# Kernel optimization log

Measured on AMD Instinct MI355X. Metric: run time of the kernel, lower is better.

## Reference

```python
import jax, jax.numpy as jnp
import numpy as np


def _apply_rope(x, rope):
    # x: (B, T, D); rope: (T, D//2, 2) broadcast over batch
    B, T, D = x.shape
    x_ = x.reshape(B, T, D // 2, 2)
    cos, sin = rope[..., 0], rope[..., 1]
    xr, xi = x_[..., 0], x_[..., 1]
    rotr = xr * cos - xi * sin
    roti = xr * sin + xi * cos
    return jnp.stack([rotr, roti], axis=-1).reshape(B, T, D)


def setup_inputs() -> dict:
    key = jax.random.key(0)
    k1, k2, k3, k4 = jax.random.split(key, 4)
    B, T, D, H = 2, 2048, 1024, 16
    x = jax.random.normal(k1, (B, T, D), dtype=jnp.float32)
    rope = jax.random.normal(k2, (T, D // 2, 2), dtype=jnp.float32)
    w_qkv = jax.random.normal(k3, (3 * D, D), dtype=jnp.float32) * (1.0 / np.sqrt(D))
    w_proj = jax.random.normal(k4, (D, D), dtype=jnp.float32) * (1.0 / np.sqrt(D))
    return {"x": x, "rope": rope, "w_qkv": w_qkv, "w_proj": w_proj}


def reference(x, rope, w_qkv, w_proj):
    B, T, D = x.shape
    H = 16
    dk = D // H
    qkv = jnp.einsum("btd,ed->bte", x, w_qkv)  # (B, T, 3D)
    q, k, v = jnp.split(qkv, 3, axis=-1)
    q = _apply_rope(q, rope)
    k = _apply_rope(k, rope)
    # split heads: (B, H, T, dk)
    q = q.reshape(B, T, H, dk).transpose(0, 2, 1, 3)
    k = k.reshape(B, T, H, dk).transpose(0, 2, 1, 3)
    v = v.reshape(B, T, H, dk).transpose(0, 2, 1, 3)
    att = jnp.einsum("bhqd,bhkd->bhqk", q, k) / jnp.sqrt(jnp.float32(dk)).astype(x.dtype)
    att = jax.nn.softmax(att, axis=-1)
    out = jnp.einsum("bhqk,bhkd->bhqd", att, v)
    out = out.transpose(0, 2, 1, 3).reshape(B, T, D)
    return jnp.einsum("btd,ed->bte", out, w_proj)
```

## Files before the change

kernel.cpp:

```cpp
#include <hip/hip_runtime.h>

typedef _Float16 f16;
typedef _Float16 f16x2 __attribute__((ext_vector_type(2)));
typedef _Float16 f16x4 __attribute__((ext_vector_type(4)));
typedef _Float16 f16x8 __attribute__((ext_vector_type(8)));
typedef float    f32x2 __attribute__((ext_vector_type(2)));
typedef float    f32x4 __attribute__((ext_vector_type(4)));
typedef short    s16x4 __attribute__((ext_vector_type(4)));

#define GLDS16(gptr, lptr)                                                     \
  __builtin_amdgcn_global_load_lds(                                            \
      (const __attribute__((address_space(1))) void*)(gptr),                   \
      (__attribute__((address_space(3))) void*)(lptr), 16, 0, 0)

#define S_BARRIER() __builtin_amdgcn_s_barrier()
#define FENCE() asm volatile("" ::: "memory")
#define WAIT_VM8() asm volatile("s_waitcnt vmcnt(8)" ::: "memory")
#define WAIT_VM0() asm volatile("s_waitcnt vmcnt(0)" ::: "memory")
#define WAIT_LGKM0() asm volatile("s_waitcnt lgkmcnt(0)" ::: "memory")

__device__ inline short f32_to_bf16_rne(float f) {
  unsigned u = __builtin_bit_cast(unsigned, f);
  return (short)((u + 0x7FFFu + ((u >> 16) & 1u)) >> 16);
}

__global__ __launch_bounds__(256) void k_cast3(const float* __restrict__ a,
                                               const float* __restrict__ b,
                                               const float* __restrict__ c,
                                               f16* __restrict__ oa,
                                               f16* __restrict__ ob,
                                               f16* __restrict__ oc) {
  int i = blockIdx.x * 256 + threadIdx.x;
  const float* src;
  f16* dst;
  int off;
  if (i < 1048576) { src = a; dst = oa; off = i; }
  else if (i < 1835008) { src = b; dst = ob; off = i - 1048576; }
  else { src = c; dst = oc; off = i - 1835008; }
  f32x4 v = ((const f32x4*)src)[off];
  f16x4 h;
  h[0] = (f16)v[0]; h[1] = (f16)v[1]; h[2] = (f16)v[2]; h[3] = (f16)v[3];
  ((f16x4*)dst)[off] = h;
}

__global__ __launch_bounds__(256, 4) void k_gemm_qkv(
    const f16* __restrict__ A, const f16* __restrict__ B,
    const float* __restrict__ rope, f16* __restrict__ qh,
    f16* __restrict__ kh, short* __restrict__ vt) {
  const int K = 1024;
  __shared__ f16 sA[128 * 64];
  __shared__ f16 sB[128 * 64];
  const int tid = threadIdx.x;
  const int wave = tid >> 6, lane = tid & 63;
  const int lr = lane & 15, lq = lane >> 4;
  const int lr7 = lr & 7;
  const int wm = (wave >> 1) * 64, wn = (wave & 1) * 64;
  const size_t m0 = (size_t)blockIdx.x * 128, n0 = (size_t)blockIdx.y * 128;

  f32x4 acc[4][4] = {};

  const int sw8 = ((tid & 7) ^ ((tid >> 3) & 7)) * 8;
  const f16* ga = A + (m0 + (tid >> 3)) * (size_t)K + sw8;
  const f16* gb = B + (n0 + (tid >> 3)) * (size_t)K + sw8;

  for (int k0 = 0; k0 < K; k0 += 64) {
    __syncthreads();
#pragma unroll
    for (int r = 0; r < 4; ++r) {
      GLDS16(ga + (size_t)(r * 32) * K + k0, (char*)sA + r * 4096 + wave * 1024);
      GLDS16(gb + (size_t)(r * 32) * K + k0, (char*)sB + r * 4096 + wave * 1024);
    }
    __syncthreads();

#pragma unroll
    for (int kk = 0; kk < 2; ++kk) {
      f16x8 af[4], bf[4];
#pragma unroll
      for (int i = 0; i < 4; ++i)
        af[i] = *(const f16x8*)&sA[(wm + i * 16 + lr) * 64 +
                                   (((kk * 4 + lq) ^ lr7) * 8)];
#pragma unroll
      for (int j = 0; j < 4; ++j)
        bf[j] = *(const f16x8*)&sB[(wn + j * 16 + lr) * 64 +
                                   (((kk * 4 + lq) ^ lr7) * 8)];
#pragma unroll
      for (int i = 0; i < 4; ++i)
#pragma unroll
        for (int j = 0; j < 4; ++j)
          acc[i][j] = __builtin_amdgcn_mfma_f32_16x16x32_f16(af[i], bf[j],
                                                             acc[i][j], 0, 0, 0);
    }
  }

  const int region = (int)(n0 >> 10);
  if (region == 2) {
#pragma unroll
    for (int i = 0; i < 4; ++i)
#pragma unroll
      for (int j = 0; j < 4; ++j) {
        int e = (int)(n0 + wn + j * 16 + lr) - 2048;
        int h = e >> 6, c = e & 63;
        int m = (int)(m0 + wm + i * 16 + lq * 4);
        int b = m >> 11, t0 = m & 2047;
        s16x4 o;
#pragma unroll
        for (int r = 0; r < 4; ++r) o[r] = f32_to_bf16_rne(acc[i][j][r]);
        *(s16x4*)&vt[(((size_t)(b * 16 + h)) * 64 + c) * 2048 + t0] = o;
      }
  } else {
    const float scl = region == 0 ? 0.1803368801111204f : 1.0f;
    f16* dst = region == 0 ? qh : kh;
    const int odd = lr & 1;
#pragma unroll
    for (int i = 0; i < 4; ++i)
#pragma unroll
      for (int j = 0; j < 4; ++j) {
        int e = ((int)(n0 + wn + j * 16 + lr)) & 1023;
        int h = e >> 6, c = e & 63, p = e >> 1;
        int mb = (int)(m0 + wm + i * 16 + lq * 4);
        int b = mb >> 11;
#pragma unroll
        for (int r = 0; r < 4; ++r) {
          int t = (mb + r) & 2047;
          float v = acc[i][j][r];
          float partner = __shfl_xor(v, 1);
          f32x2 cs = *(const f32x2*)&rope[((size_t)t * 512 + p) * 2];
          float out = odd ? (partner * cs[1] + v * cs[0])
                          : (v * cs[0] - partner * cs[1]);
          dst[(((size_t)(b * 16 + h)) * 2048 + t) * 64 + c] = (f16)(out * scl);
        }
      }
  }
}

__global__ __launch_bounds__(256, 4) void k_gemm_bt(const f16* __restrict__ A,
                                                    const f16* __restrict__ B,
                                                    float* __restrict__ C,
                                                    int M, int N, int K) {
  __shared__ f16 sA[128 * 64];
  __shared__ f16 sB[128 * 64];
  const int tid = threadIdx.x;
  const int wave = tid >> 6, lane = tid & 63;
  const int lr = lane & 15, lq = lane >> 4;
  const int lr7 = lr & 7;
  const int wm = (wave >> 1) * 64, wn = (wave & 1) * 64;
  const size_t m0 = (size_t)blockIdx.x * 128, n0 = (size_t)blockIdx.y * 128;

  f32x4 acc[4][4] = {};

  const int sw8 = ((tid & 7) ^ ((tid >> 3) & 7)) * 8;
  const f16* ga = A + (m0 + (tid >> 3)) * (size_t)K + sw8;
  const f16* gb = B + (n0 + (tid >> 3)) * (size_t)K + sw8;

  for (int k0 = 0; k0 < K; k0 += 64) {
    __syncthreads();
#pragma unroll
    for (int r = 0; r < 4; ++r) {
      GLDS16(ga + (size_t)(r * 32) * K + k0, (char*)sA + r * 4096 + wave * 1024);
      GLDS16(gb + (size_t)(r * 32) * K + k0, (char*)sB + r * 4096 + wave * 1024);
    }
    __syncthreads();

#pragma unroll
    for (int kk = 0; kk < 2; ++kk) {
      f16x8 af[4], bf[4];
#pragma unroll
      for (int i = 0; i < 4; ++i)
        af[i] = *(const f16x8*)&sA[(wm + i * 16 + lr) * 64 +
                                   (((kk * 4 + lq) ^ lr7) * 8)];
#pragma unroll
      for (int j = 0; j < 4; ++j)
        bf[j] = *(const f16x8*)&sB[(wn + j * 16 + lr) * 64 +
                                   (((kk * 4 + lq) ^ lr7) * 8)];
#pragma unroll
      for (int i = 0; i < 4; ++i)
#pragma unroll
        for (int j = 0; j < 4; ++j)
          acc[i][j] = __builtin_amdgcn_mfma_f32_16x16x32_f16(af[i], bf[j],
                                                             acc[i][j], 0, 0, 0);
    }
  }

#pragma unroll
  for (int i = 0; i < 4; ++i)
#pragma unroll
    for (int j = 0; j < 4; ++j)
#pragma unroll
      for (int r = 0; r < 4; ++r)
        C[(m0 + wm + i * 16 + lq * 4 + r) * (size_t)N + n0 + wn + j * 16 + lr] =
            acc[i][j][r];
}

__global__ __launch_bounds__(256, 2) void k_attn(const f16* __restrict__ Qp,
                                                 const f16* __restrict__ Kp,
                                                 const short* __restrict__ Vt,
                                                 f16* __restrict__ Op) {
  __shared__ f16 sQ[128 * 64];
  __shared__ f16 sKV[2 * 16384];
  const int tid = threadIdx.x, wave = tid >> 6, lane = tid & 63;
  const int lr = lane & 15, lq = lane >> 4;
  const int lr7 = lr & 7;
  const int bh = blockIdx.x, qt = blockIdx.y;
  const size_t base = (size_t)bh * 2048 * 64;

  const int sw8 = ((tid & 7) ^ ((tid >> 3) & 7)) * 8;
  const int sw16 = ((tid & 15) ^ ((tid >> 4) & 15)) * 8;

  auto stage_kv = [&](int jcc, int d) {
    const f16* gk = Kp + base + (size_t)jcc * 128 * 64;
    const short* gv = Vt + base + (size_t)jcc * 128;
    char* bK = (char*)sKV + d * 32768;
    char* bV = bK + 16384;
#pragma unroll
    for (int r = 0; r < 4; ++r) {
      GLDS16(gk + (size_t)(r * 32 + (tid >> 3)) * 64 + sw8,
             bK + r * 4096 + wave * 1024);
      GLDS16(gv + (size_t)(r * 16 + (tid >> 4)) * 2048 + sw16,
             bV + r * 4096 + wave * 1024);
    }
  };

  const f16* gq = Qp + base + (size_t)qt * 128 * 64;
#pragma unroll
  for (int r = 0; r < 4; ++r)
    GLDS16(gq + (size_t)(r * 32 + (tid >> 3)) * 64 + sw8,
           (char*)sQ + r * 4096 + wave * 1024);
  stage_kv(0, 0);
  WAIT_VM8();
  S_BARRIER();
  FENCE();
  f16x8 qa0 = *(const f16x8*)&sQ[(wave * 32 + lr) * 64 + ((lq ^ lr7) * 8)];
  f16x8 qa1 = *(const f16x8*)&sQ[(wave * 32 + lr) * 64 + (((4 + lq) ^ lr7) * 8)];
  f16x8 qb0 = *(const f16x8*)&sQ[(wave * 32 + 16 + lr) * 64 + ((lq ^ lr7) * 8)];
  f16x8 qb1 =
      *(const f16x8*)&sQ[(wave * 32 + 16 + lr) * 64 + (((4 + lq) ^ lr7) * 8)];

  f32x4 ota[4] = {}, otb[4] = {};
  float la = 0.f, lb = 0.f;

#pragma unroll 1
  for (int jc = 0; jc < 16; ++jc) {
    const int cur = jc & 1;
    if (jc < 15) {
      stage_kv(jc + 1, cur ^ 1);
      WAIT_VM8();
    } else {
      WAIT_VM0();
    }
    S_BARRIER();
    FENCE();

    const f16* bK = (const f16*)((char*)sKV + cur * 32768);
    const short* bV = (const short*)((char*)sKV + cur * 32768 + 16384);

    s16x4 pfa[8], pfb[8];
#pragma unroll
    for (int nt = 0; nt < 8; ++nt) {
      f16x8 kf0 = *(const f16x8*)&bK[(nt * 16 + lr) * 64 + ((lq ^ lr7) * 8)];
      f16x8 kf1 =
          *(const f16x8*)&bK[(nt * 16 + lr) * 64 + (((4 + lq) ^ lr7) * 8)];
      f32x4 z = {0.f, 0.f, 0.f, 0.f};
      f32x4 sa = __builtin_amdgcn_mfma_f32_16x16x32_f16(kf0, qa0, z, 0, 0, 0);
      sa = __builtin_amdgcn_mfma_f32_16x16x32_f16(kf1, qa1, sa, 0, 0, 0);
      f32x4 sb = __builtin_amdgcn_mfma_f32_16x16x32_f16(kf0, qb0, z, 0, 0, 0);
      sb = __builtin_amdgcn_mfma_f32_16x16x32_f16(kf1, qb1, sb, 0, 0, 0);
#pragma unroll
      for (int r = 0; r < 4; ++r) {
        float pa = __builtin_amdgcn_exp2f(sa[r]);
        float pb = __builtin_amdgcn_exp2f(sb[r]);
        la += pa; lb += pb;
        pfa[nt][r] = (short)(__builtin_bit_cast(unsigned, pa) >> 16);
        pfb[nt][r] = (short)(__builtin_bit_cast(unsigned, pb) >> 16);
      }
    }

#pragma unroll
    for (int d = 0; d < 4; ++d)
#pragma unroll
      for (int ks = 0; ks < 8; ++ks) {
        int vslot = (ks * 2 + (lq >> 1)) ^ lr;
        s16x4 vf = *(const s16x4*)&bV[(d * 16 + lr) * 128 + vslot * 8 +
                                      (lq & 1) * 4];
        ota[d] = __builtin_amdgcn_mfma_f32_16x16x16bf16_1k(vf, pfa[ks], ota[d],
                                                           0, 0, 0);
        otb[d] = __builtin_amdgcn_mfma_f32_16x16x16bf16_1k(vf, pfb[ks], otb[d],
                                                           0, 0, 0);
      }

    WAIT_LGKM0();
    S_BARRIER();
    FENCE();
  }

  la += __shfl_xor(la, 16); la += __shfl_xor(la, 32);
  lb += __shfl_xor(lb, 16); lb += __shfl_xor(lb, 32);
  float rla = 1.f / la, rlb = 1.f / lb;
  int b = bh >> 4, h = bh & 15;
  int ta = qt * 128 + wave * 32 + lr;
  f16* gouta = Op + ((size_t)(b * 2048 + ta)) * 1024 + h * 64;
  f16* goutb = gouta + (size_t)16 * 1024;
#pragma unroll
  for (int d = 0; d < 4; ++d) {
    f16x4 oa, ob;
#pragma unroll
    for (int r = 0; r < 4; ++r) {
      oa[r] = (f16)(ota[d][r] * rla);
      ob[r] = (f16)(otb[d][r] * rlb);
    }
    *(f16x4*)&gouta[d * 16 + lq * 4] = oa;
    *(f16x4*)&goutb[d * 16 + lq * 4] = ob;
  }
}

extern "C" void kernel_launch(void* const* d_in, const int* in_sizes, int n_in,
                              void* d_out, int out_size, void* d_ws,
                              size_t ws_size, hipStream_t stream) {
  const float* x     = (const float*)d_in[0];
  const float* rope  = (const float*)d_in[1];
  const float* wqkv  = (const float*)d_in[2];
  const float* wproj = (const float*)d_in[3];
  float* out = (float*)d_out;

  char* w = (char*)d_ws;
  const size_t MB = 1024 * 1024;
  f16* xh   = (f16*)(w + 0);
  f16* wqh  = (f16*)(w + 8 * MB);
  f16* wph  = (f16*)(w + 14 * MB);
  f16* qh   = (f16*)(w + 16 * MB);
  f16* kh   = (f16*)(w + 24 * MB);
  short* vth = (short*)(w + 32 * MB);
  f16* aoh  = (f16*)(w + 40 * MB);

  k_cast3<<<8192, 256, 0, stream>>>(x, wqkv, wproj, xh, wqh, wph);

  k_gemm_qkv<<<dim3(32, 24), 256, 0, stream>>>(xh, wqh, rope, qh, kh, vth);

  k_attn<<<dim3(32, 16), 256, 0, stream>>>(qh, kh, vth, aoh);

  k_gemm_bt<<<dim3(32, 8), 256, 0, stream>>>(aoh, wph, out, 4096, 1024, 1024);
}
```

Baseline: 193.8 us.

## Split attention Q tile across eight waves with sixteen query rows each

The attention kernel now launches 512 threads per block, and each of the eight waves handles 16 query rows instead of 32. The KV staging loads are redistributed across the larger thread count and the vmcnt wait threshold is adjusted to match. This halves per-wave register use (accumulators and P fragments), with the aim of more waves in flight and better latency hiding. In exchange, each K/V fragment read from LDS is reused by half as many MFMAs, so LDS read traffic per FLOP doubles.

```diff
diff --git a/kernel.cpp b/kernel.cpp
--- a/kernel.cpp
+++ b/kernel.cpp
@@ -15,7 +15,7 @@
 
 #define S_BARRIER() __builtin_amdgcn_s_barrier()
 #define FENCE() asm volatile("" ::: "memory")
-#define WAIT_VM8() asm volatile("s_waitcnt vmcnt(8)" ::: "memory")
+#define WAIT_VM4() asm volatile("s_waitcnt vmcnt(4)" ::: "memory")
 #define WAIT_VM0() asm volatile("s_waitcnt vmcnt(0)" ::: "memory")
 #define WAIT_LGKM0() asm volatile("s_waitcnt lgkmcnt(0)" ::: "memory")
 
@@ -191,7 +191,7 @@
             acc[i][j][r];
 }
 
-__global__ __launch_bounds__(256, 2) void k_attn(const f16* __restrict__ Qp,
+__global__ __launch_bounds__(512, 4) void k_attn(const f16* __restrict__ Qp,
                                                  const f16* __restrict__ Kp,
                                                  const short* __restrict__ Vt,
                                                  f16* __restrict__ Op) {
@@ -212,38 +212,36 @@
     char* bK = (char*)sKV + d * 32768;
     char* bV = bK + 16384;
 #pragma unroll
-    for (int r = 0; r < 4; ++r) {
-      GLDS16(gk + (size_t)(r * 32 + (tid >> 3)) * 64 + sw8,
-             bK + r * 4096 + wave * 1024);
-      GLDS16(gv + (size_t)(r * 16 + (tid >> 4)) * 2048 + sw16,
-             bV + r * 4096 + wave * 1024);
+    for (int r = 0; r < 2; ++r) {
+      GLDS16(gk + (size_t)(r * 64 + (tid >> 3)) * 64 + sw8,
+             bK + r * 8192 + wave * 1024);
+      GLDS16(gv + (size_t)(r * 32 + (tid >> 4)) * 2048 + sw16,
+             bV + r * 8192 + wave * 1024);
     }
   };
 
   const f16* gq = Qp + base + (size_t)qt * 128 * 64;
 #pragma unroll
-  for (int r = 0; r < 4; ++r)
-    GLDS16(gq + (size_t)(r * 32 + (tid >> 3)) * 64 + sw8,
-           (char*)sQ + r * 4096 + wave * 1024);
+  for (int r = 0; r < 2; ++r)
+    GLDS16(gq + (size_t)(r * 64 + (tid >> 3)) * 64 + sw8,
+           (char*)sQ + r * 8192 + wave * 1024);
   stage_kv(0, 0);
-  WAIT_VM8();
+  WAIT_VM4();
   S_BARRIER();
   FENCE();
-  f16x8 qa0 = *(const f16x8*)&sQ[(wave * 32 + lr) * 64 + ((lq ^ lr7) * 8)];
-  f16x8 qa1 = *(const f16x8*)&sQ[(wave * 32 + lr) * 64 + (((4 + lq) ^ lr7) * 8)];
-  f16x8 qb0 = *(const f16x8*)&sQ[(wave * 32 + 16 + lr) * 64 + ((lq ^ lr7) * 8)];
-  f16x8 qb1 =
-      *(const f16x8*)&sQ[(wave * 32 + 16 + lr) * 64 + (((4 + lq) ^ lr7) * 8)];
-
-  f32x4 ota[4] = {}, otb[4] = {};
-  float la = 0.f, lb = 0.f;
+  const int qrow = wave * 16 + lr;
+  f16x8 qa0 = *(const f16x8*)&sQ[qrow * 64 + ((lq ^ lr7) * 8)];
+  f16x8 qa1 = *(const f16x8*)&sQ[qrow * 64 + (((4 + lq) ^ lr7) * 8)];
+
+  f32x4 ot[4] = {};
+  float la = 0.f;
 
 #pragma unroll 1
   for (int jc = 0; jc < 16; ++jc) {
     const int cur = jc & 1;
     if (jc < 15) {
       stage_kv(jc + 1, cur ^ 1);
-      WAIT_VM8();
+      WAIT_VM4();
     } else {
       WAIT_VM0();
     }
@@ -253,7 +251,7 @@
     const f16* bK = (const f16*)((char*)sKV + cur * 32768);
     const short* bV = (const short*)((char*)sKV + cur * 32768 + 16384);
 
-    s16x4 pfa[8], pfb[8];
+    s16x4 pf[8];
 #pragma unroll
     for (int nt = 0; nt < 8; ++nt) {
       f16x8 kf0 = *(const f16x8*)&bK[(nt * 16 + lr) * 64 + ((lq ^ lr7) * 8)];
@@ -262,15 +260,11 @@
       f32x4 z = {0.f, 0.f, 0.f, 0.f};
       f32x4 sa = __builtin_amdgcn_mfma_f32_16x16x32_f16(kf0, qa0, z, 0, 0, 0);
       sa = __builtin_amdgcn_mfma_f32_16x16x32_f16(kf1, qa1, sa, 0, 0, 0);
-      f32x4 sb = __builtin_amdgcn_mfma_f32_16x16x32_f16(kf0, qb0, z, 0, 0, 0);
-      sb = __builtin_amdgcn_mfma_f32_16x16x32_f16(kf1, qb1, sb, 0, 0, 0);
 #pragma unroll
       for (int r = 0; r < 4; ++r) {
         float pa = __builtin_amdgcn_exp2f(sa[r]);
-        float pb = __builtin_amdgcn_exp2f(sb[r]);
-        la += pa; lb += pb;
-        pfa[nt][r] = (short)(__builtin_bit_cast(unsigned, pa) >> 16);
-        pfb[nt][r] = (short)(__builtin_bit_cast(unsigned, pb) >> 16);
+        la += pa;
+        pf[nt][r] = (short)(__builtin_bit_cast(unsigned, pa) >> 16);
       }
     }
 
@@ -281,10 +275,8 @@
         int vslot = (ks * 2 + (lq >> 1)) ^ lr;
         s16x4 vf = *(const s16x4*)&bV[(d * 16 + lr) * 128 + vslot * 8 +
                                       (lq & 1) * 4];
-        ota[d] = __builtin_amdgcn_mfma_f32_16x16x16bf16_1k(vf, pfa[ks], ota[d],
-                                                           0, 0, 0);
-        otb[d] = __builtin_amdgcn_mfma_f32_16x16x16bf16_1k(vf, pfb[ks], otb[d],
-                                                           0, 0, 0);
+        ot[d] = __builtin_amdgcn_mfma_f32_16x16x16bf16_1k(vf, pf[ks], ot[d],
+                                                          0, 0, 0);
       }
 
     WAIT_LGKM0();
@@ -293,22 +285,16 @@
   }
 
   la += __shfl_xor(la, 16); la += __shfl_xor(la, 32);
-  lb += __shfl_xor(lb, 16); lb += __shfl_xor(lb, 32);
-  float rla = 1.f / la, rlb = 1.f / lb;
+  float rla = 1.f / la;
   int b = bh >> 4, h = bh & 15;
-  int ta = qt * 128 + wave * 32 + lr;
-  f16* gouta = Op + ((size_t)(b * 2048 + ta)) * 1024 + h * 64;
-  f16* goutb = gouta + (size_t)16 * 1024;
+  int ta = qt * 128 + wave * 16 + lr;
+  f16* gout = Op + ((size_t)(b * 2048 + ta)) * 1024 + h * 64;
 #pragma unroll
   for (int d = 0; d < 4; ++d) {
-    f16x4 oa, ob;
-#pragma unroll
-    for (int r = 0; r < 4; ++r) {
-      oa[r] = (f16)(ota[d][r] * rla);
-      ob[r] = (f16)(otb[d][r] * rlb);
-    }
-    *(f16x4*)&gouta[d * 16 + lq * 4] = oa;
-    *(f16x4*)&goutb[d * 16 + lq * 4] = ob;
+    f16x4 oa;
+#pragma unroll
+    for (int r = 0; r < 4; ++r) oa[r] = (f16)(ot[d][r] * rla);
+    *(f16x4*)&gout[d * 16 + lq * 4] = oa;
   }
 }
 
@@ -335,7 +321,7 @@
 
   k_gemm_qkv<<<dim3(32, 24), 256, 0, stream>>>(xh, wqh, rope, qh, kh, vth);
 
-  k_attn<<<dim3(32, 16), 256, 0, stream>>>(qh, kh, vth, aoh);
+  k_attn<<<dim3(32, 16), 512, 0, stream>>>(qh, kh, vth, aoh);
 
   k_gemm_bt<<<dim3(32, 8), 256, 0, stream>>>(aoh, wph, out, 4096, 1024, 1024);
 }
```

New measurement: 198.1 us. 2.2% more time.
